# Performance work log

Measured on AMD Instinct MI355X. Metric: run time of the kernel, lower is better.

## Reference

```python
import jax, jax.numpy as jnp
import numpy as np

DIM = 256
HEADS = 8
DIM_HEAD = 32
WS = 8  # window_size
INNER = HEADS * DIM_HEAD
SCALE = DIM_HEAD ** -0.5


def _rel_indices():
    # (WS^2, WS^2, 2) relative position indices, shifted to be non-negative
    idx = np.array([[x, y] for x in range(WS) for y in range(WS)])
    rel = idx[None, :, :] - idx[:, None, :] + (WS - 1)
    return jnp.asarray(rel, dtype=jnp.int32)


def setup_inputs() -> dict:
    key = jax.random.key(0)
    k1, k2, k3, k4 = jax.random.split(key, 4)
    x = jax.random.normal(k1, (2, 4, 128, 128, DIM), dtype=jnp.float32)
    w_qkv = jax.random.normal(k2, (DIM, 3 * INNER), dtype=jnp.float32) * 0.02
    pos_emb = jax.random.normal(k3, (2 * WS - 1, 2 * WS - 1), dtype=jnp.float32)
    w_out = jax.random.normal(k4, (INNER, DIM), dtype=jnp.float32) * 0.02
    b_out = jnp.zeros((DIM,), dtype=jnp.float32)
    return {"x": x, "w_qkv": w_qkv, "pos_emb": pos_emb, "w_out": w_out, "b_out": b_out}


def reference(x, w_qkv, pos_emb, w_out, b_out):
    B, L, H, W, C = x.shape
    nh, nw = H // WS, W // WS
    qkv = x @ w_qkv  # (B,L,H,W,3*INNER)
    q, k, v = jnp.split(qkv, 3, axis=-1)

    def to_windows(t):
        # (B,L,H,W,INNER) -> (B,L,m,nh*nw,WS*WS,DIM_HEAD)
        t = t.reshape(B, L, nh, WS, nw, WS, HEADS, DIM_HEAD)
        t = t.transpose(0, 1, 6, 2, 4, 3, 5, 7)
        return t.reshape(B, L, HEADS, nh * nw, WS * WS, DIM_HEAD)

    q, k, v = to_windows(q), to_windows(k), to_windows(v)

    rel = _rel_indices()
    bias = pos_emb[rel[..., 0], rel[..., 1]]  # (WS^2, WS^2)

    dots = jnp.einsum('blmhic,blmhjc->blmhij', q, k) * SCALE + bias
    attn = jax.nn.softmax(dots, axis=-1)
    out = jnp.einsum('blmhij,blmhjc->blmhic', attn, v)

    # inverse window rearrange: (B,L,m,nh*nw,WS*WS,c) -> (B,L,H,W,INNER)
    out = out.reshape(B, L, HEADS, nh, nw, WS, WS, DIM_HEAD)
    out = out.transpose(0, 1, 3, 5, 4, 6, 2, 7).reshape(B, L, H, W, INNER)
    return out @ w_out + b_out
```

## Files before the change

### kernel.cpp

```cpp
#include <hip/hip_runtime.h>
#include <hip/hip_bf16.h>


typedef __attribute__((ext_vector_type(8))) short bf16x8;
typedef __attribute__((ext_vector_type(4))) float f32x4;

__device__ __forceinline__ f32x4 mfma16(bf16x8 a, bf16x8 b, f32x4 c) {
  return __builtin_amdgcn_mfma_f32_16x16x32_bf16(a, b, c, 0, 0, 0);
}

__device__ __forceinline__ unsigned short f2bf(float f) {
  __hip_bfloat16 h = __float2bfloat16(f);
  return *reinterpret_cast<unsigned short*>(&h);
}

__device__ __forceinline__ uint2 pack4(float a, float b, float c, float d) {
  union { unsigned short u[4]; uint2 v; } pk;
  pk.u[0] = f2bf(a); pk.u[1] = f2bf(b); pk.u[2] = f2bf(c); pk.u[3] = f2bf(d);
  return pk.v;
}

#define LOG2E 1.4426950408889634f
#define EXPSCALE (0.17677669529663687f * 1.4426950408889634f)

#define XSTR 264
#define VSTR 72
#define SSTR 72
#define OFF_A  0
#define OFF_B  18432
#define OFF_SC 35328
#define SMEM_ELTS 39936

__global__ void prep_kernel(const float* __restrict__ w_qkv,
                            const float* __restrict__ w_out,
                            const float* __restrict__ pos_emb,
                            unsigned short* __restrict__ wqkvT,
                            unsigned short* __restrict__ woutT,
                            float* __restrict__ bias64) {
  const int stride = gridDim.x * blockDim.x;
  const int tid = blockIdx.x * blockDim.x + threadIdx.x;
  for (int i = tid; i < 768 * 256; i += stride) {
    int n = i >> 8, k = i & 255;
    int off = ((((n >> 4) * 8 + (k >> 5)) * 4 + ((k >> 3) & 3)) * 16 + (n & 15)) * 8 + (k & 7);
    wqkvT[off] = f2bf(w_qkv[k * 768 + n]);
  }
  for (int i = tid; i < 256 * 256; i += stride) {
    int n = i >> 8, k = i & 255;
    int off = ((((n >> 4) * 8 + (k >> 5)) * 4 + ((k >> 3) & 3)) * 16 + (n & 15)) * 8 + (k & 7);
    woutT[off] = f2bf(w_out[k * 256 + n]);
  }
  for (int i = tid; i < 64 * 64; i += stride) {
    int a = i >> 6, b = i & 63;
    int d0 = (b >> 3) - (a >> 3) + 7;
    int d1 = (b & 7) - (a & 7) + 7;
    bias64[i] = pos_emb[d0 * 15 + d1] * LOG2E;
  }
}

template <bool SWAP>
__device__ __forceinline__ void qkv_gemm(f32x4 (&acc)[4][4],
                                         const unsigned short* __restrict__ x_lds,
                                         const unsigned short* __restrict__ wqkvT,
                                         int col0, int l15, int lq, int swz) {
  const f32x4 zero4 = {0.f, 0.f, 0.f, 0.f};
#pragma unroll
  for (int rt = 0; rt < 4; ++rt)
#pragma unroll
    for (int ct = 0; ct < 4; ++ct) acc[rt][ct] = zero4;

  bf16x8 aP[4], bP[4], aN[4], bN[4];
#pragma unroll
  for (int rt = 0; rt < 4; ++rt)
    aP[rt] = *(const bf16x8*)&x_lds[(rt * 16 + l15) * XSTR + ((lq * 8) ^ swz)];
#pragma unroll
  for (int ct = 0; ct < 4; ++ct)
    bP[ct] = *(const bf16x8*)&wqkvT[(((col0 >> 4) + ct) * 32 + lq) * 128 + l15 * 8];
#pragma unroll
  for (int kk = 0; kk < 8; ++kk) {
    if (kk < 7) {
      const int ko = ((kk + 1) * 32 + lq * 8) ^ swz;
#pragma unroll
      for (int rt = 0; rt < 4; ++rt)
        aN[rt] = *(const bf16x8*)&x_lds[(rt * 16 + l15) * XSTR + ko];
#pragma unroll
      for (int ct = 0; ct < 4; ++ct)
        bN[ct] = *(const bf16x8*)&wqkvT[((((col0 >> 4) + ct) * 8 + kk + 1) * 4 + lq) * 128 + l15 * 8];
    }
#pragma unroll
    for (int rt = 0; rt < 4; ++rt)
#pragma unroll
      for (int ct = 0; ct < 4; ++ct)
        acc[rt][ct] = SWAP ? mfma16(bP[ct], aP[rt], acc[rt][ct])
                           : mfma16(aP[rt], bP[ct], acc[rt][ct]);
#pragma unroll
    for (int rt = 0; rt < 4; ++rt) aP[rt] = aN[rt];
#pragma unroll
    for (int ct = 0; ct < 4; ++ct) bP[ct] = bN[ct];
  }
}

__global__ __launch_bounds__(256, 2)
void winattn_kernel(const float* __restrict__ x,
                    const unsigned short* __restrict__ wqkvT,
                    const unsigned short* __restrict__ woutT,
                    const float* __restrict__ bias64,
                    const float* __restrict__ b_out,
                    float* __restrict__ out) {
  __shared__ unsigned short smem[SMEM_ELTS];

  const int tid = threadIdx.x;
  const int lane = tid & 63;
  const int w = tid >> 6;
  const int l15 = lane & 15;
  const int lq = lane >> 4;
  const int swz = (l15 & 7) << 3;

  const int bid = blockIdx.x;
  const int win = bid & 255;
  const int img = bid >> 8;
  const int wy = win >> 4, wx = win & 15;

  unsigned short* x_lds  = smem + OFF_A;
  unsigned short* vT_lds = smem + OFF_A;
  unsigned short* qk_lds = smem + OFF_B;
  unsigned short* sc = smem + OFF_SC + w * (16 * SSTR);

  const f32x4 zero4 = {0.f, 0.f, 0.f, 0.f};
  const size_t img_base = (size_t)img * 128 * 128 * 256;

  {
#pragma unroll
    for (int r = 0; r < 16; ++r) {
      int p = r * 4 + w;
      const float* src = x + img_base +
          (((size_t)(wy * 8 + (p >> 3)) * 128) + (wx * 8 + (p & 7))) * 256 + lane * 4;
      float4 v4 = *(const float4*)src;
      *(uint2*)&x_lds[p * XSTR + ((lane * 4) ^ ((p & 7) << 3))] =
          pack4(v4.x, v4.y, v4.z, v4.w);
    }
  }
  __syncthreads();

  {
    f32x4 acc[4][4];
    qkv_gemm<true>(acc, x_lds, wqkvT, w * 64, l15, lq, swz);
#pragma unroll
    for (int rt = 0; rt < 4; ++rt)
#pragma unroll
      for (int ct = 0; ct < 4; ++ct)
        *(uint2*)&qk_lds[(rt * 16 + l15) * XSTR + ((w * 64 + ct * 16 + lq * 4) ^ swz)] =
            pack4(acc[rt][ct][0], acc[rt][ct][1], acc[rt][ct][2], acc[rt][ct][3]);
  }
  __syncthreads();

  bf16x8 qf[8];
#pragma unroll
  for (int h = 0; h < 8; ++h)
    qf[h] = *(const bf16x8*)&qk_lds[(w * 16 + l15) * XSTR + ((h * 32 + lq * 8) ^ swz)];

  {
    f32x4 kacc[4][4];
    qkv_gemm<true>(kacc, x_lds, wqkvT, 256 + w * 64, l15, lq, swz);
    __syncthreads();
#pragma unroll
    for (int rt = 0; rt < 4; ++rt)
#pragma unroll
      for (int ct = 0; ct < 4; ++ct)
        *(uint2*)&qk_lds[(rt * 16 + l15) * XSTR + ((w * 64 + ct * 16 + lq * 4) ^ swz)] =
            pack4(kacc[rt][ct][0], kacc[rt][ct][1], kacc[rt][ct][2], kacc[rt][ct][3]);
  }

  {
    f32x4 vacc[4][4];
    qkv_gemm<false>(vacc, x_lds, wqkvT, 512 + w * 64, l15, lq, swz);
    __syncthreads();
#pragma unroll
    for (int rt = 0; rt < 4; ++rt)
#pragma unroll
      for (int ct = 0; ct < 4; ++ct)
        *(uint2*)&vT_lds[(w * 64 + ct * 16 + l15) * VSTR + ((rt * 16 + lq * 4) ^ swz)] =
            pack4(vacc[rt][ct][0], vacc[rt][ct][1], vacc[rt][ct][2], vacc[rt][ct][3]);
  }
  __syncthreads();

  f32x4 bias4[4];
#pragma unroll
  for (int rt = 0; rt < 4; ++rt)
    bias4[rt] = *(const f32x4*)&bias64[(w * 16 + l15) * 64 + rt * 16 + lq * 4];

  const short one_bf = (short)0x3F80;
  const bf16x8 ones = {one_bf, one_bf, one_bf, one_bf,
                       one_bf, one_bf, one_bf, one_bf};

  f32x4 ACC[16];
#pragma unroll
  for (int ct = 0; ct < 16; ++ct) ACC[ct] = zero4;

  f32x4 s_t[4];
#pragma unroll
  for (int rt = 0; rt < 4; ++rt) {
    const bf16x8 bk = *(const bf16x8*)&qk_lds[(rt * 16 + l15) * XSTR + ((lq * 8) ^ swz)];
    f32x4 t = mfma16(bk, qf[0], zero4);
#pragma unroll
    for (int r = 0; r < 4; ++r)
      s_t[rt][r] = __builtin_amdgcn_exp2f(t[r] * EXPSCALE + bias4[rt][r]);
  }

#pragma unroll
  for (int h = 0; h < 8; ++h) {
#pragma unroll
    for (int rt = 0; rt < 4; ++rt)
      *(uint2*)&sc[l15 * SSTR + ((rt * 16 + lq * 4) ^ swz)] =
          pack4(s_t[rt][0], s_t[rt][1], s_t[rt][2], s_t[rt][3]);

    f32x4 sn[4];
    if (h < 7) {
#pragma unroll
      for (int rt = 0; rt < 4; ++rt) {
        const bf16x8 bk = *(const bf16x8*)&qk_lds[(rt * 16 + l15) * XSTR + (((h + 1) * 32 + lq * 8) ^ swz)];
        f32x4 t = mfma16(bk, qf[h + 1], zero4);
#pragma unroll
        for (int r = 0; r < 4; ++r)
          sn[rt][r] = __builtin_amdgcn_exp2f(t[r] * EXPSCALE + bias4[rt][r]);
      }
    }

    const bf16x8 ap0 = *(const bf16x8*)&sc[l15 * SSTR + ((lq * 8) ^ swz)];
    const bf16x8 ap1 = *(const bf16x8*)&sc[l15 * SSTR + ((32 + lq * 8) ^ swz)];
    bf16x8 bw[16];
#pragma unroll
    for (int ct = 0; ct < 16; ++ct)
      bw[ct] = *(const bf16x8*)&woutT[((ct * 8 + h) * 4 + lq) * 128 + l15 * 8];

    f32x4 o0 = zero4, o1 = zero4, osum = zero4;
    {
      const bf16x8 bv00 = *(const bf16x8*)&vT_lds[(h * 32 + l15) * VSTR + ((lq * 8) ^ swz)];
      const bf16x8 bv01 = *(const bf16x8*)&vT_lds[(h * 32 + l15) * VSTR + ((32 + lq * 8) ^ swz)];
      const bf16x8 bv10 = *(const bf16x8*)&vT_lds[(h * 32 + 16 + l15) * VSTR + ((lq * 8) ^ swz)];
      const bf16x8 bv11 = *(const bf16x8*)&vT_lds[(h * 32 + 16 + l15) * VSTR + ((32 + lq * 8) ^ swz)];
      o0 = mfma16(bv00, ap0, o0);  o0 = mfma16(bv01, ap1, o0);
      o1 = mfma16(bv10, ap0, o1);  o1 = mfma16(bv11, ap1, o1);
      osum = mfma16(ones, ap0, osum);
      osum = mfma16(ones, ap1, osum);
    }

    const float rinv = __builtin_amdgcn_rcpf(osum[0]);
    *(uint2*)&sc[l15 * SSTR + ((lq * 4) ^ swz)] =
        pack4(o0[0] * rinv, o0[1] * rinv, o0[2] * rinv, o0[3] * rinv);
    *(uint2*)&sc[l15 * SSTR + ((16 + lq * 4) ^ swz)] =
        pack4(o1[0] * rinv, o1[1] * rinv, o1[2] * rinv, o1[3] * rinv);

    const bf16x8 ao = *(const bf16x8*)&sc[l15 * SSTR + ((lq * 8) ^ swz)];
#pragma unroll
    for (int ct = 0; ct < 16; ++ct)
      ACC[ct] = mfma16(ao, bw[ct], ACC[ct]);

    if (h < 7) {
#pragma unroll
      for (int rt = 0; rt < 4; ++rt) s_t[rt] = sn[rt];
    }
  }

  {
#pragma unroll
    for (int ct = 0; ct < 16; ++ct) {
      const int n = ct * 16 + l15;
      const float bo = b_out[n];
#pragma unroll
      for (int r = 0; r < 4; ++r) {
        const int p = w * 16 + lq * 4 + r;
        const size_t off = img_base +
            (((size_t)(wy * 8 + (p >> 3)) * 128) + (wx * 8 + (p & 7))) * 256 + n;
        out[off] = ACC[ct][r] + bo;
      }
    }
  }
}

extern "C" void kernel_launch(void* const* d_in, const int* in_sizes, int n_in,
                              void* d_out, int out_size, void* d_ws, size_t ws_size,
                              hipStream_t stream) {
  const float* x       = (const float*)d_in[0];
  const float* w_qkv   = (const float*)d_in[1];
  const float* pos_emb = (const float*)d_in[2];
  const float* w_out   = (const float*)d_in[3];
  const float* b_out   = (const float*)d_in[4];
  float* out = (float*)d_out;

  unsigned short* wqkvT = (unsigned short*)d_ws;
  unsigned short* woutT = wqkvT + 768 * 256;
  float* bias64 = (float*)(woutT + 256 * 256);

  prep_kernel<<<96, 256, 0, stream>>>(w_qkv, w_out, pos_emb, wqkvT, woutT, bias64);
  winattn_kernel<<<2048, 256, 0, stream>>>(x, wqkvT, woutT, bias64, b_out, out);
}
```

Measured before the change: 142.2 us.

## Drop LDS XOR swizzle and vectorize output stores via transposed MFMA

Removes the XOR swizzle from every LDS index, so shared-memory rows are addressed linearly. It also swaps the MFMA operand order in the output projection, so each lane holds four consecutive output columns of one pixel. The epilogue can then issue 16-byte float4 stores and bias loads instead of scalar stores. The swizzle removal saves address arithmetic but risks LDS bank conflicts, depending on the XSTR/SSTR/VSTR padding.

```diff
diff --git a/kernel.cpp b/kernel.cpp
--- a/kernel.cpp
+++ b/kernel.cpp
@@ -61,7 +61,7 @@
 __device__ __forceinline__ void qkv_gemm(f32x4 (&acc)[4][4],
                                          const unsigned short* __restrict__ x_lds,
                                          const unsigned short* __restrict__ wqkvT,
-                                         int col0, int l15, int lq, int swz) {
+                                         int col0, int l15, int lq) {
   const f32x4 zero4 = {0.f, 0.f, 0.f, 0.f};
 #pragma unroll
   for (int rt = 0; rt < 4; ++rt)
@@ -71,14 +71,14 @@
   bf16x8 aP[4], bP[4], aN[4], bN[4];
 #pragma unroll
   for (int rt = 0; rt < 4; ++rt)
-    aP[rt] = *(const bf16x8*)&x_lds[(rt * 16 + l15) * XSTR + ((lq * 8) ^ swz)];
+    aP[rt] = *(const bf16x8*)&x_lds[(rt * 16 + l15) * XSTR + lq * 8];
 #pragma unroll
   for (int ct = 0; ct < 4; ++ct)
     bP[ct] = *(const bf16x8*)&wqkvT[(((col0 >> 4) + ct) * 32 + lq) * 128 + l15 * 8];
 #pragma unroll
   for (int kk = 0; kk < 8; ++kk) {
     if (kk < 7) {
-      const int ko = ((kk + 1) * 32 + lq * 8) ^ swz;
+      const int ko = (kk + 1) * 32 + lq * 8;
 #pragma unroll
       for (int rt = 0; rt < 4; ++rt)
         aN[rt] = *(const bf16x8*)&x_lds[(rt * 16 + l15) * XSTR + ko];
@@ -113,7 +113,6 @@
   const int w = tid >> 6;
   const int l15 = lane & 15;
   const int lq = lane >> 4;
-  const int swz = (l15 & 7) << 3;
 
   const int bid = blockIdx.x;
   const int win = bid & 255;
@@ -135,20 +134,19 @@
       const float* src = x + img_base +
           (((size_t)(wy * 8 + (p >> 3)) * 128) + (wx * 8 + (p & 7))) * 256 + lane * 4;
       float4 v4 = *(const float4*)src;
-      *(uint2*)&x_lds[p * XSTR + ((lane * 4) ^ ((p & 7) << 3))] =
-          pack4(v4.x, v4.y, v4.z, v4.w);
+      *(uint2*)&x_lds[p * XSTR + lane * 4] = pack4(v4.x, v4.y, v4.z, v4.w);
     }
   }
   __syncthreads();
 
   {
     f32x4 acc[4][4];
-    qkv_gemm<true>(acc, x_lds, wqkvT, w * 64, l15, lq, swz);
-#pragma unroll
-    for (int rt = 0; rt < 4; ++rt)
-#pragma unroll
-      for (int ct = 0; ct < 4; ++ct)
-        *(uint2*)&qk_lds[(rt * 16 + l15) * XSTR + ((w * 64 + ct * 16 + lq * 4) ^ swz)] =
+    qkv_gemm<true>(acc, x_lds, wqkvT, w * 64, l15, lq);
+#pragma unroll
+    for (int rt = 0; rt < 4; ++rt)
+#pragma unroll
+      for (int ct = 0; ct < 4; ++ct)
+        *(uint2*)&qk_lds[(rt * 16 + l15) * XSTR + w * 64 + ct * 16 + lq * 4] =
             pack4(acc[rt][ct][0], acc[rt][ct][1], acc[rt][ct][2], acc[rt][ct][3]);
   }
   __syncthreads();
@@ -156,29 +154,29 @@
   bf16x8 qf[8];
 #pragma unroll
   for (int h = 0; h < 8; ++h)
-    qf[h] = *(const bf16x8*)&qk_lds[(w * 16 + l15) * XSTR + ((h * 32 + lq * 8) ^ swz)];
+    qf[h] = *(const bf16x8*)&qk_lds[(w * 16 + l15) * XSTR + h * 32 + lq * 8];
 
   {
     f32x4 kacc[4][4];
-    qkv_gemm<true>(kacc, x_lds, wqkvT, 256 + w * 64, l15, lq, swz);
+    qkv_gemm<true>(kacc, x_lds, wqkvT, 256 + w * 64, l15, lq);
     __syncthreads();
 #pragma unroll
     for (int rt = 0; rt < 4; ++rt)
 #pragma unroll
       for (int ct = 0; ct < 4; ++ct)
-        *(uint2*)&qk_lds[(rt * 16 + l15) * XSTR + ((w * 64 + ct * 16 + lq * 4) ^ swz)] =
+        *(uint2*)&qk_lds[(rt * 16 + l15) * XSTR + w * 64 + ct * 16 + lq * 4] =
             pack4(kacc[rt][ct][0], kacc[rt][ct][1], kacc[rt][ct][2], kacc[rt][ct][3]);
   }
 
   {
     f32x4 vacc[4][4];
-    qkv_gemm<false>(vacc, x_lds, wqkvT, 512 + w * 64, l15, lq, swz);
+    qkv_gemm<false>(vacc, x_lds, wqkvT, 512 + w * 64, l15, lq);
     __syncthreads();
 #pragma unroll
     for (int rt = 0; rt < 4; ++rt)
 #pragma unroll
       for (int ct = 0; ct < 4; ++ct)
-        *(uint2*)&vT_lds[(w * 64 + ct * 16 + l15) * VSTR + ((rt * 16 + lq * 4) ^ swz)] =
+        *(uint2*)&vT_lds[(w * 64 + ct * 16 + l15) * VSTR + rt * 16 + lq * 4] =
             pack4(vacc[rt][ct][0], vacc[rt][ct][1], vacc[rt][ct][2], vacc[rt][ct][3]);
   }
   __syncthreads();
@@ -199,7 +197,7 @@
   f32x4 s_t[4];
 #pragma unroll
   for (int rt = 0; rt < 4; ++rt) {
-    const bf16x8 bk = *(const bf16x8*)&qk_lds[(rt * 16 + l15) * XSTR + ((lq * 8) ^ swz)];
+    const bf16x8 bk = *(const bf16x8*)&qk_lds[(rt * 16 + l15) * XSTR + lq * 8];
     f32x4 t = mfma16(bk, qf[0], zero4);
 #pragma unroll
     for (int r = 0; r < 4; ++r)
@@ -210,14 +208,14 @@
   for (int h = 0; h < 8; ++h) {
 #pragma unroll
     for (int rt = 0; rt < 4; ++rt)
-      *(uint2*)&sc[l15 * SSTR + ((rt * 16 + lq * 4) ^ swz)] =
+      *(uint2*)&sc[l15 * SSTR + rt * 16 + lq * 4] =
           pack4(s_t[rt][0], s_t[rt][1], s_t[rt][2], s_t[rt][3]);
 
     f32x4 sn[4];
     if (h < 7) {
 #pragma unroll
       for (int rt = 0; rt < 4; ++rt) {
-        const bf16x8 bk = *(const bf16x8*)&qk_lds[(rt * 16 + l15) * XSTR + (((h + 1) * 32 + lq * 8) ^ swz)];
+        const bf16x8 bk = *(const bf16x8*)&qk_lds[(rt * 16 + l15) * XSTR + (h + 1) * 32 + lq * 8];
         f32x4 t = mfma16(bk, qf[h + 1], zero4);
 #pragma unroll
         for (int r = 0; r < 4; ++r)
@@ -225,8 +223,8 @@
       }
     }
 
-    const bf16x8 ap0 = *(const bf16x8*)&sc[l15 * SSTR + ((lq * 8) ^ swz)];
-    const bf16x8 ap1 = *(const bf16x8*)&sc[l15 * SSTR + ((32 + lq * 8) ^ swz)];
+    const bf16x8 ap0 = *(const bf16x8*)&sc[l15 * SSTR + lq * 8];
+    const bf16x8 ap1 = *(const bf16x8*)&sc[l15 * SSTR + 32 + lq * 8];
     bf16x8 bw[16];
 #pragma unroll
     for (int ct = 0; ct < 16; ++ct)
@@ -234,10 +232,10 @@
 
     f32x4 o0 = zero4, o1 = zero4, osum = zero4;
     {
-      const bf16x8 bv00 = *(const bf16x8*)&vT_lds[(h * 32 + l15) * VSTR + ((lq * 8) ^ swz)];
-      const bf16x8 bv01 = *(const bf16x8*)&vT_lds[(h * 32 + l15) * VSTR + ((32 + lq * 8) ^ swz)];
-      const bf16x8 bv10 = *(const bf16x8*)&vT_lds[(h * 32 + 16 + l15) * VSTR + ((lq * 8) ^ swz)];
-      const bf16x8 bv11 = *(const bf16x8*)&vT_lds[(h * 32 + 16 + l15) * VSTR + ((32 + lq * 8) ^ swz)];
+      const bf16x8 bv00 = *(const bf16x8*)&vT_lds[(h * 32 + l15) * VSTR + lq * 8];
+      const bf16x8 bv01 = *(const bf16x8*)&vT_lds[(h * 32 + l15) * VSTR + 32 + lq * 8];
+      const bf16x8 bv10 = *(const bf16x8*)&vT_lds[(h * 32 + 16 + l15) * VSTR + lq * 8];
+      const bf16x8 bv11 = *(const bf16x8*)&vT_lds[(h * 32 + 16 + l15) * VSTR + 32 + lq * 8];
       o0 = mfma16(bv00, ap0, o0);  o0 = mfma16(bv01, ap1, o0);
       o1 = mfma16(bv10, ap0, o1);  o1 = mfma16(bv11, ap1, o1);
       osum = mfma16(ones, ap0, osum);
@@ -245,15 +243,15 @@
     }
 
     const float rinv = __builtin_amdgcn_rcpf(osum[0]);
-    *(uint2*)&sc[l15 * SSTR + ((lq * 4) ^ swz)] =
+    *(uint2*)&sc[l15 * SSTR + lq * 4] =
         pack4(o0[0] * rinv, o0[1] * rinv, o0[2] * rinv, o0[3] * rinv);
-    *(uint2*)&sc[l15 * SSTR + ((16 + lq * 4) ^ swz)] =
+    *(uint2*)&sc[l15 * SSTR + 16 + lq * 4] =
         pack4(o1[0] * rinv, o1[1] * rinv, o1[2] * rinv, o1[3] * rinv);
 
-    const bf16x8 ao = *(const bf16x8*)&sc[l15 * SSTR + ((lq * 8) ^ swz)];
+    const bf16x8 ao = *(const bf16x8*)&sc[l15 * SSTR + lq * 8];
 #pragma unroll
     for (int ct = 0; ct < 16; ++ct)
-      ACC[ct] = mfma16(ao, bw[ct], ACC[ct]);
+      ACC[ct] = mfma16(bw[ct], ao, ACC[ct]);
 
     if (h < 7) {
 #pragma unroll
@@ -262,17 +260,17 @@
   }
 
   {
+    const int p = w * 16 + l15;
+    float* orow = out + img_base +
+        (((size_t)(wy * 8 + (p >> 3)) * 128) + (wx * 8 + (p & 7))) * 256;
 #pragma unroll
     for (int ct = 0; ct < 16; ++ct) {
-      const int n = ct * 16 + l15;
-      const float bo = b_out[n];
-#pragma unroll
-      for (int r = 0; r < 4; ++r) {
-        const int p = w * 16 + lq * 4 + r;
-        const size_t off = img_base +
-            (((size_t)(wy * 8 + (p >> 3)) * 128) + (wx * 8 + (p & 7))) * 256 + n;
-        out[off] = ACC[ct][r] + bo;
-      }
+      const int n0 = ct * 16 + lq * 4;
+      const f32x4 bo4 = *(const f32x4*)&b_out[n0];
+      f32x4 st;
+#pragma unroll
+      for (int r = 0; r < 4; ++r) st[r] = ACC[ct][r] + bo4[r];
+      *(f32x4*)(orow + n0) = st;
     }
   }
 }
```

Result: faster. 132.4 us (-6.9%).
